# Performance work log

Hardware: AMD Instinct MI355X
Metric: run time of the kernel (lower is better)

Reference implementation:

```python
import jax, jax.numpy as jnp
import numpy as np

B, L, D = 2, 2048, 512
P, M = 32, 1024          # persistent slots, neural-memory slots
H, HD = 8, 64            # heads, head_dim (H*HD == D)
WIN = 256
EPS = 1e-5


def _layer_norm(x, g, b):
    mu = jnp.mean(x, axis=-1, keepdims=True)
    var = jnp.mean(jnp.square(x - mu), axis=-1, keepdims=True)
    return (x - mu) * jax.lax.rsqrt(var + EPS) * g + b


def setup_inputs() -> dict:
    key = jax.random.key(0)
    ks = jax.random.split(key, 12)
    s = 1.0 / np.sqrt(D)
    f32 = jnp.float32
    return {
        "x": jax.random.normal(ks[0], (B, L, D), f32),
        "persistent_memory": jax.random.normal(ks[1], (P, D), f32),
        "mem_keys": jax.random.normal(ks[2], (M, D), f32) * s,
        "mem_Wk": jax.random.normal(ks[3], (D, D), f32) * s,
        "mem_Wv": jax.random.normal(ks[4], (D, D), f32) * s,
        "mem_Wq": jax.random.normal(ks[5], (D, D), f32) * s,
        "attn_Wq": jax.random.normal(ks[6], (D, H * HD), f32) * s,
        "attn_Wk": jax.random.normal(ks[7], (D, H * HD), f32) * s,
        "attn_Wv": jax.random.normal(ks[8], (D, H * HD), f32) * s,
        "attn_Wo": jax.random.normal(ks[9], (H * HD, D), f32) * s,
        "ln1_g": jnp.ones((D,), f32), "ln1_b": jnp.zeros((D,), f32),
        "ln2_g": jnp.ones((D,), f32), "ln2_b": jnp.zeros((D,), f32),
        "out_W": jax.random.normal(ks[10], (D, D), f32) * s,
        "out_b": jnp.zeros((D,), f32),
    }


def reference(x, persistent_memory, mem_keys, mem_Wk, mem_Wv, mem_Wq,
              attn_Wq, attn_Wk, attn_Wv, attn_Wo,
              ln1_g, ln1_b, ln2_g, ln2_b, out_W, out_b):
    b = x.shape[0]
    # --- persistent memory concat: (B, S, D), S = P + L ---
    pm = jnp.broadcast_to(persistent_memory[None], (b, P, D))
    combined = jnp.concatenate([pm, x], axis=1)
    S = combined.shape[1]

    # --- NeuralMemory: write (update) then read (retrieve) ---
    k = combined @ mem_Wk                                   # (B,S,D)
    v = combined @ mem_Wv                                   # (B,S,D)
    w_write = jax.nn.softmax(jnp.einsum('bsd,md->bsm', k, mem_keys), axis=-1)
    state = jnp.einsum('bsm,bsd->bmd', w_write, v)          # zeros init + scatter-write
    q = combined @ mem_Wq
    w_read = jax.nn.softmax(jnp.einsum('bsd,md->bsm', q, mem_keys), axis=-1)
    mem_out = jnp.einsum('bsm,bmd->bsd', w_read, state)     # (B,S,D)

    h = _layer_norm(mem_out, ln1_g, ln1_b)

    # --- sliding-window multi-head attention ---
    qh = (h @ attn_Wq).reshape(b, S, H, HD)
    kh = (h @ attn_Wk).reshape(b, S, H, HD)
    vh = (h @ attn_Wv).reshape(b, S, H, HD)
    scores = jnp.einsum('bqhd,bkhd->bhqk', qh, kh) / np.sqrt(HD)
    idx = jnp.arange(S)
    band = jnp.abs(idx[:, None] - idx[None, :]) < WIN       # (S,S) local band
    scores = jnp.where(band[None, None], scores, jnp.finfo(scores.dtype).min)
    attn = jax.nn.softmax(scores, axis=-1)
    ao = jnp.einsum('bhqk,bkhd->bqhd', attn, vh).reshape(b, S, H * HD)
    ao = ao @ attn_Wo

    ao = _layer_norm(ao, ln2_g, ln2_b)
    return ao @ out_W + out_b
```

## Files before the change

### kernel.cpp

```cpp
#include <hip/hip_runtime.h>
#include <hip/hip_bf16.h>

#define B_ 2
#define L_ 2048
#define D_ 512
#define P_ 32
#define M_ 1024
#define H_ 8
#define HD_ 64
#define WIN_ 256
#define S_ (P_ + L_)
#define N_ (B_ * S_)

typedef __hip_bfloat16 bf16;
typedef __attribute__((ext_vector_type(8))) short short8;
typedef __attribute__((ext_vector_type(4))) short short4_t;
typedef __attribute__((ext_vector_type(4))) float f32x4;

__device__ __forceinline__ int imin(int a, int b) { return a < b ? a : b; }
__device__ __forceinline__ int imax(int a, int b) { return a > b ? a : b; }

__device__ __forceinline__ float ld_in(const void* p, long i, int f32) {
    return f32 ? ((const float*)p)[i]
               : __bfloat162float(((const bf16*)p)[i]);
}

__device__ __forceinline__ short bfbits(float f) {
    bf16 h = __float2bfloat16(f);
    short s;
    __builtin_memcpy(&s, &h, 2);
    return s;
}

__device__ __forceinline__ float b2f(short s) {
    unsigned int u = ((unsigned int)(unsigned short)s) << 16;
    float f;
    __builtin_memcpy(&f, &u, 4);
    return f;
}

__device__ __forceinline__ void gload_lds16(const void* g, void* l) {
    __builtin_amdgcn_global_load_lds(
        (const __attribute__((address_space(1))) unsigned int*)g,
        (__attribute__((address_space(3))) unsigned int*)l, 16, 0, 0);
}

#define F_X   0
#define F_PM  1
#define F_MK  2
#define F_WK  3
#define F_OW  10

__global__ __launch_bounds__(256) void detect_kernel(
    const void* a0, const void* a1, const void* a2, const void* a3,
    const void* a4, const void* a5, const void* a6, const void* a7,
    const void* a8, const void* a9, const void* a10, int* __restrict__ flags)
{
    const void* p;
    switch (blockIdx.x) {
        case 0: p = a0; break;  case 1: p = a1; break;
        case 2: p = a2; break;  case 3: p = a3; break;
        case 4: p = a4; break;  case 5: p = a5; break;
        case 6: p = a6; break;  case 7: p = a7; break;
        case 8: p = a8; break;  case 9: p = a9; break;
        default: p = a10; break;
    }
    const unsigned short* u = (const unsigned short*)p;
    __shared__ int c;
    if (threadIdx.x == 0) c = 0;
    __syncthreads();
    int cnt = 0;
    #pragma unroll
    for (int i = 0; i < 8; ++i) {
        unsigned short v = u[(threadIdx.x << 3) + i];
        cnt += (((v >> 7) & 0xFF) >= 0xC0) ? 1 : 0;
    }
    atomicAdd(&c, cnt);
    __syncthreads();
    if (threadIdx.x == 0) flags[blockIdx.x] = (c >= 8) ? 1 : 0;
}

struct Ptr8 { const void* p[8]; };

__global__ __launch_bounds__(256) void prep_kernel(
    const void* __restrict__ x, const void* __restrict__ pm,
    const void* __restrict__ mk, Ptr8 wptrs,
    bf16* __restrict__ comb, bf16* __restrict__ mkbf, bf16* __restrict__ WT,
    const int* __restrict__ flags)
{
    const int blk = blockIdx.x;
    const int tid = threadIdx.x;
    if (blk < 8320) {
        const int fx = flags[F_X];
        const int fp = flags[F_PM];
        int i = blk * 256 + tid;
        int d = i & (D_ - 1);
        int r = i >> 9;
        int s = r % S_;
        int b = r / S_;
        float v;
        if (s < P_) v = ld_in(pm, (long)s * D_ + d, fp);
        else        v = ld_in(x, ((long)(b * L_ + (s - P_))) * D_ + d, fx);
        comb[i] = __float2bfloat16(v);
        return;
    }
    if (blk < 10368) {
        const int f = flags[F_MK];
        int i = (blk - 8320) * 256 + tid;
        mkbf[i] = __float2bfloat16(ld_in(mk, i, f));
        return;
    }
    __shared__ short T[64][65];
    const int t = blk - 10368;
    const int widx = t >> 6;
    const int rem = t & 63;
    const int r0 = (rem >> 3) * 64, c0 = (rem & 7) * 64;
    const void* in = wptrs.p[widx];
    const int flag = flags[F_WK + widx];
    short* o = (short*)(WT + (long)widx * 512 * 512);
    #pragma unroll
    for (int i = 0; i < 2; ++i) {
        int ch = tid + i * 256;
        int r = ch >> 3, c8 = (ch & 7) * 8;
        long base = (long)(r0 + r) * 512 + c0 + c8;
        if (flag) {
            const float4 f0 = *reinterpret_cast<const float4*>((const float*)in + base);
            const float4 f1 = *reinterpret_cast<const float4*>((const float*)in + base + 4);
            T[r][c8+0]=bfbits(f0.x); T[r][c8+1]=bfbits(f0.y); T[r][c8+2]=bfbits(f0.z); T[r][c8+3]=bfbits(f0.w);
            T[r][c8+4]=bfbits(f1.x); T[r][c8+5]=bfbits(f1.y); T[r][c8+6]=bfbits(f1.z); T[r][c8+7]=bfbits(f1.w);
        } else {
            const short8 v = *reinterpret_cast<const short8*>((const short*)in + base);
            #pragma unroll
            for (int k = 0; k < 8; ++k) T[r][c8+k] = v[k];
        }
    }
    __syncthreads();
    #pragma unroll
    for (int i = 0; i < 2; ++i) {
        int ch = tid + i * 256;
        int n = ch >> 3, c8 = (ch & 7) * 8;
        #pragma unroll
        for (int k = 0; k < 8; ++k)
            o[(long)(c0 + n) * 512 + r0 + c8 + k] = T[c8 + k][n];
    }
}

__global__ __launch_bounds__(256) void transpose_b_kernel(
    const bf16* __restrict__ in_, bf16* __restrict__ out_, int R, int C)
{
    const short* in = (const short*)(in_ + (long)blockIdx.z * R * C);
    short* out = (short*)(out_ + (long)blockIdx.z * C * R);
    __shared__ short T[64][65];
    const int r0 = blockIdx.y * 64, c0 = blockIdx.x * 64;
    const int tid = threadIdx.x;
    #pragma unroll
    for (int i = 0; i < 2; ++i) {
        int ch = tid + i * 256;
        int r = ch >> 3, c8 = (ch & 7) * 8;
        int row = imin(r0 + r, R - 1);
        const short8 v = *reinterpret_cast<const short8*>(in + (long)row * C + c0 + c8);
        #pragma unroll
        for (int k = 0; k < 8; ++k) T[r][c8+k] = v[k];
    }
    __syncthreads();
    #pragma unroll
    for (int i = 0; i < 2; ++i) {
        int ch = tid + i * 256;
        int n = ch >> 3, c8 = (ch & 7) * 8;
        #pragma unroll
        for (int k = 0; k < 8; ++k) {
            int col = r0 + c8 + k;
            if (col < R) out[(long)(c0 + n) * R + col] = T[c8 + k][n];
        }
    }
}

template<int CMODE, int BN, int UN>
__global__ __launch_bounds__(256, 4) void gemm64(
    const bf16* __restrict__ A, const bf16* __restrict__ Bb,
    void* __restrict__ C0, void* __restrict__ C1, void* __restrict__ C2,
    const int* __restrict__ flags,
    int Mdim, int Kdim, int lda, int ldb, int ldc,
    long sA, long sB, long sC, int SK)
{
    constexpr int NH = BN / 64;
    __shared__ __align__(16) bf16 As[UN * 2048];
    __shared__ __align__(16) bf16 Bs[UN * BN * 32];
    const int tid = threadIdx.x, lane = tid & 63, wid = tid >> 6;
    constexpr int WNc = BN / 4;
    constexpr int NJ = WNc / 16;
    const int m0 = blockIdx.y * 64, n0 = blockIdx.x * BN;
    const int z = blockIdx.z;
    const int bz = z / SK, kc = z - bz * SK;
    const int kLen = Kdim / SK;
    const int kBeg = kc * kLen;
    const bf16* Ab = A + (long)bz * sA;
    const bf16* Bp = Bb + (long)bz * sB;

    const int sRow = tid >> 2, c8 = (tid & 3) * 8;
    int aRow = m0 + sRow;
    if (aRow >= Mdim) aRow = Mdim - 1;
    const bf16* aS = Ab + (long)aRow * lda + c8 + kBeg;
    const bf16* bS[NH];
    #pragma unroll
    for (int h = 0; h < NH; ++h)
        bS[h] = Bp + (long)(n0 + sRow + h * 64) * ldb + c8 + kBeg;

    const int g8 = (lane >> 4) * 8, l15 = lane & 15;
    f32x4 acc[4][NJ] = {};

    for (int k0 = 0; k0 < kLen; k0 += UN * 32) {
        #pragma unroll
        for (int t = 0; t < UN; ++t) {
            gload_lds16(aS + k0 + t * 32, As + t * 2048 + wid * 512);
            #pragma unroll
            for (int h = 0; h < NH; ++h)
                gload_lds16(bS[h] + k0 + t * 32, Bs + t * BN * 32 + h * 2048 + wid * 512);
        }
        __syncthreads();
        #pragma unroll
        for (int t = 0; t < UN; ++t) {
            short8 af[4], bfr[NJ];
            #pragma unroll
            for (int mi = 0; mi < 4; ++mi)
                af[mi] = *reinterpret_cast<const short8*>(
                    &As[t * 2048 + (mi * 16 + l15) * 32 + g8]);
            #pragma unroll
            for (int nj = 0; nj < NJ; ++nj)
                bfr[nj] = *reinterpret_cast<const short8*>(
                    &Bs[t * BN * 32 + (wid * WNc + nj * 16 + l15) * 32 + g8]);
            #pragma unroll
            for (int mi = 0; mi < 4; ++mi)
                #pragma unroll
                for (int nj = 0; nj < NJ; ++nj)
                    acc[mi][nj] = __builtin_amdgcn_mfma_f32_16x16x32_bf16(
                        af[mi], bfr[nj], acc[mi][nj], 0, 0, 0);
        }
        __syncthreads();
    }

    const int oflag = (CMODE == 2) ? flags[F_OW] : 0;
    const int grp = n0 >> 9;
    #pragma unroll
    for (int mi = 0; mi < 4; ++mi) {
        #pragma unroll
        for (int nj = 0; nj < NJ; ++nj) {
            #pragma unroll
            for (int r = 0; r < 4; ++r) {
                int row = m0 + mi * 16 + (lane >> 4) * 4 + r;
                int col = n0 + wid * WNc + nj * 16 + l15;
                if (row >= Mdim) continue;
                float val = acc[mi][nj][r];
                if (CMODE == 0) {
                    ((float*)C0)[(long)z * sC + (long)row * ldc + col] = val;
                } else if (CMODE == 1) {
                    ((bf16*)C0)[(long)z * sC + (long)row * ldc + col] = __float2bfloat16(val);
                } else if (CMODE == 2) {
                    long idx = (long)row * 512 + col;
                    if (oflag) ((float*)C0)[idx] = val;
                    else       ((bf16*)C0)[idx] = __float2bfloat16(val);
                } else if (CMODE == 6) {
                    int b = row / S_, s = row - b * S_;
                    int c = col - (grp << 9);
                    if (grp == 0)      ((bf16*)C0)[(long)row * 512 + c] = __float2bfloat16(val);
                    else if (grp == 1) ((bf16*)C1)[((long)b * 512 + c) * S_ + s] = __float2bfloat16(val);
                    else               ((bf16*)C2)[(long)row * 512 + c] = __float2bfloat16(val);
                } else {
                    int b = row / S_, s = row - b * S_;
                    int c = col - (grp << 9);
                    int h = c >> 6, d = c & 63;
                    if (grp == 0)      ((bf16*)C0)[((long)(b * H_ + h) * S_ + s) * HD_ + d] = __float2bfloat16(val);
                    else if (grp == 1) ((bf16*)C1)[((long)(b * H_ + h) * S_ + s) * HD_ + d] = __float2bfloat16(val);
                    else               ((bf16*)C2)[((long)(b * H_ + h) * HD_ + d) * S_ + s] = __float2bfloat16(val);
                }
            }
        }
    }
}

__global__ __launch_bounds__(256) void reduce_state_kernel(
    const bf16* __restrict__ P, bf16* __restrict__ stT)
{
    long g = ((long)blockIdx.x * 256 + threadIdx.x) * 8;
    int b = (int)(g >> 19);
    long dm = g & ((1L << 19) - 1);
    float s[8] = {};
    #pragma unroll
    for (int c = 0; c < 5; ++c) {
        const short8 v = *reinterpret_cast<const short8*>(
            (const short*)P + (((long)(b * 5 + c)) << 19) + dm);
        #pragma unroll
        for (int k = 0; k < 8; ++k) s[k] += b2f(v[k]);
    }
    short8 o;
    #pragma unroll
    for (int k = 0; k < 8; ++k) o[k] = bfbits(s[k]);
    *reinterpret_cast<short8*>((short*)stT + g) = o;
}

__global__ __launch_bounds__(256) void softmax_rows_kernel(
    const bf16* __restrict__ w, bf16* __restrict__ o)
{
    const int row = blockIdx.x;
    const int tid = threadIdx.x;
    const short4_t v4 = *reinterpret_cast<const short4_t*>(
        (const short*)w + (long)row * M_ + (tid << 2));
    float vx = b2f(v4[0]), vy = b2f(v4[1]), vz = b2f(v4[2]), vw = b2f(v4[3]);
    float mx = fmaxf(fmaxf(vx, vy), fmaxf(vz, vw));
    #pragma unroll
    for (int off = 32; off > 0; off >>= 1) mx = fmaxf(mx, __shfl_xor(mx, off, 64));
    __shared__ float rmax[4];
    __shared__ float rsum[4];
    const int wid = tid >> 6;
    if ((tid & 63) == 0) rmax[wid] = mx;
    __syncthreads();
    mx = fmaxf(fmaxf(rmax[0], rmax[1]), fmaxf(rmax[2], rmax[3]));
    float ex = __expf(vx - mx), ey = __expf(vy - mx);
    float ez = __expf(vz - mx), ew = __expf(vw - mx);
    float s = ex + ey + ez + ew;
    #pragma unroll
    for (int off = 32; off > 0; off >>= 1) s += __shfl_xor(s, off, 64);
    if ((tid & 63) == 0) rsum[wid] = s;
    __syncthreads();
    s = rsum[0] + rsum[1] + rsum[2] + rsum[3];
    const float inv = 1.f / s;
    short4_t ob;
    ob[0] = bfbits(ex * inv); ob[1] = bfbits(ey * inv);
    ob[2] = bfbits(ez * inv); ob[3] = bfbits(ew * inv);
    *reinterpret_cast<short4_t*>((short*)o + (long)row * M_ + (tid << 2)) = ob;
}

__global__ __launch_bounds__(256) void layernorm_kernel(
    const bf16* __restrict__ x, bf16* __restrict__ o)
{
    const int row = blockIdx.x;
    const int tid = threadIdx.x;
    const short* p = (const short*)x + (long)row * D_;
    float v0 = b2f(p[tid]), v1 = b2f(p[tid + 256]);
    float s  = v0 + v1;
    float sq = v0 * v0 + v1 * v1;
    #pragma unroll
    for (int off = 32; off > 0; off >>= 1) {
        s  += __shfl_xor(s,  off, 64);
        sq += __shfl_xor(sq, off, 64);
    }
    __shared__ float rs[4];
    __shared__ float rq[4];
    const int wid = tid >> 6;
    if ((tid & 63) == 0) { rs[wid] = s; rq[wid] = sq; }
    __syncthreads();
    s  = rs[0] + rs[1] + rs[2] + rs[3];
    sq = rq[0] + rq[1] + rq[2] + rq[3];
    const float mu  = s * (1.f / D_);
    const float var = sq * (1.f / D_) - mu * mu;
    const float inv = rsqrtf(var + 1e-5f);
    bf16* ob = o + (long)row * D_;
    ob[tid]       = __float2bfloat16((v0 - mu) * inv);
    ob[tid + 256] = __float2bfloat16((v1 - mu) * inv);
}

__global__ __launch_bounds__(256) void flash_attn_kernel(
    const bf16* __restrict__ qh, const bf16* __restrict__ kh,
    const bf16* __restrict__ vhT, bf16* __restrict__ ao)
{
    const int qt = blockIdx.x, h = blockIdx.y, b = blockIdx.z;
    const int tid = threadIdx.x, w = tid >> 6, lane = tid & 63;
    const int g = lane >> 4, l15 = lane & 15, g8 = g * 8;
    const int q0 = qt * 64;
    __shared__ __align__(16) bf16 Qs[64 * 72];
    __shared__ __align__(16) bf16 Ks[64 * 72];
    __shared__ __align__(16) bf16 Vs[64 * 72];
    __shared__ __align__(16) bf16 Ps[4 * 16 * 88];
    const long bh = (long)(b * H_ + h);
    const bf16* qb = qh + bh * S_ * HD_;
    const bf16* kb = kh + bh * S_ * HD_;
    const bf16* vb = vhT + bh * HD_ * S_;

    #pragma unroll
    for (int i = 0; i < 2; ++i) {
        int ch = tid + i * 256;
        int r = ch >> 3, c8 = (ch & 7) * 8;
        int q = imin(q0 + r, S_ - 1);
        *reinterpret_cast<short8*>(&Qs[r * 72 + c8]) =
            *reinterpret_cast<const short8*>(qb + (long)q * HD_ + c8);
    }
    float mrow[4] = {-1e20f, -1e20f, -1e20f, -1e20f};
    float lrow[4] = {};
    f32x4 O[4] = {};
    const int tstart = imax(0, q0 - (WIN_ - 1)) >> 6;
    const int tend = imin(S_ - 1, q0 + 63 + (WIN_ - 1)) >> 6;

    for (int jt = tstart; jt <= tend; ++jt) {
        __syncthreads();
        #pragma unroll
        for (int i = 0; i < 2; ++i) {
            int ch = tid + i * 256;
            int r = ch >> 3, c8 = (ch & 7) * 8;
            int j = imin(jt * 64 + r, S_ - 1);
            *reinterpret_cast<short8*>(&Ks[r * 72 + c8]) =
                *reinterpret_cast<const short8*>(kb + (long)j * HD_ + c8);
            int jc = jt * 64 + c8;
            if (jc + 8 <= S_) {
                *reinterpret_cast<short8*>(&Vs[r * 72 + c8]) =
                    *reinterpret_cast<const short8*>(vb + (long)r * S_ + jc);
            } else {
                short8 v;
                #pragma unroll
                for (int k = 0; k < 8; ++k)
                    v[k] = ((const short*)vb)[(long)r * S_ + imin(jc + k, S_ - 1)];
                *reinterpret_cast<short8*>(&Vs[r * 72 + c8]) = v;
            }
        }
        __syncthreads();
        f32x4 s[4] = {};
        const short8 aq0 = *reinterpret_cast<const short8*>(&Qs[(w * 16 + l15) * 72 + g8]);
        const short8 aq1 = *reinterpret_cast<const short8*>(&Qs[(w * 16 + l15) * 72 + 32 + g8]);
        #pragma unroll
        for (int nj = 0; nj < 4; ++nj) {
            const short8 b0 = *reinterpret_cast<const short8*>(&Ks[(nj * 16 + l15) * 72 + g8]);
            const short8 b1 = *reinterpret_cast<const short8*>(&Ks[(nj * 16 + l15) * 72 + 32 + g8]);
            s[nj] = __builtin_amdgcn_mfma_f32_16x16x32_bf16(aq0, b0, s[nj], 0, 0, 0);
            s[nj] = __builtin_amdgcn_mfma_f32_16x16x32_bf16(aq1, b1, s[nj], 0, 0, 0);
        }
        #pragma unroll
        for (int nj = 0; nj < 4; ++nj) {
            int j = jt * 64 + nj * 16 + l15;
            #pragma unroll
            for (int r = 0; r < 4; ++r) {
                int q = q0 + w * 16 + g * 4 + r;
                int dd = q - j;
                bool ok = (dd > -WIN_) && (dd < WIN_) && (q < S_) && (j < S_);
                s[nj][r] = ok ? s[nj][r] * 0.125f : -1e30f;
            }
        }
        float alpha[4];
        #pragma unroll
        for (int r = 0; r < 4; ++r) {
            float mt = fmaxf(fmaxf(s[0][r], s[1][r]), fmaxf(s[2][r], s[3][r]));
            #pragma unroll
            for (int off = 8; off; off >>= 1) mt = fmaxf(mt, __shfl_xor(mt, off, 64));
            float mnew = fmaxf(mrow[r], mt);
            alpha[r] = __expf(mrow[r] - mnew);
            mrow[r] = mnew;
            float ps = 0.f;
            #pragma unroll
            for (int nj = 0; nj < 4; ++nj) {
                float pv = __expf(s[nj][r] - mnew);
                s[nj][r] = pv;
                ps += pv;
            }
            #pragma unroll
            for (int off = 8; off; off >>= 1) ps += __shfl_xor(ps, off, 64);
            lrow[r] = lrow[r] * alpha[r] + ps;
        }
        #pragma unroll
        for (int nj = 0; nj < 4; ++nj) {
            #pragma unroll
            for (int r = 0; r < 4; ++r) {
                Ps[w * 1408 + (g * 4 + r) * 88 + nj * 16 + l15] = __float2bfloat16(s[nj][r]);
                O[nj][r] *= alpha[r];
            }
        }
        __syncthreads();
        const short8 ap0 = *reinterpret_cast<const short8*>(&Ps[w * 1408 + l15 * 88 + g8]);
        const short8 ap1 = *reinterpret_cast<const short8*>(&Ps[w * 1408 + l15 * 88 + 32 + g8]);
        #pragma unroll
        for (int nj = 0; nj < 4; ++nj) {
            const short8 b0 = *reinterpret_cast<const short8*>(&Vs[(nj * 16 + l15) * 72 + g8]);
            const short8 b1 = *reinterpret_cast<const short8*>(&Vs[(nj * 16 + l15) * 72 + 32 + g8]);
            O[nj] = __builtin_amdgcn_mfma_f32_16x16x32_bf16(ap0, b0, O[nj], 0, 0, 0);
            O[nj] = __builtin_amdgcn_mfma_f32_16x16x32_bf16(ap1, b1, O[nj], 0, 0, 0);
        }
    }
    float inv[4];
    #pragma unroll
    for (int r = 0; r < 4; ++r) inv[r] = lrow[r] > 0.f ? 1.f / lrow[r] : 0.f;
    #pragma unroll
    for (int nj = 0; nj < 4; ++nj) {
        #pragma unroll
        for (int r = 0; r < 4; ++r) {
            int q = q0 + w * 16 + g * 4 + r;
            if (q < S_)
                ao[((long)b * S_ + q) * D_ + h * HD_ + nj * 16 + l15] =
                    __float2bfloat16(O[nj][r] * inv[r]);
        }
    }
}

extern "C" void kernel_launch(void* const* d_in, const int* in_sizes, int n_in,
                              void* d_out, int out_size, void* d_ws, size_t ws_size,
                              hipStream_t stream)
{
    const void* x        = d_in[0];
    const void* pm       = d_in[1];
    const void* mem_keys = d_in[2];

    char* wsb = (char*)d_ws;
    bf16*  comb  = (bf16*)(wsb + 0x0);
    bf16*  kbf   = (bf16*)(wsb + 0x410000);
    bf16*  qbf   = (bf16*)(wsb + 0x820000);
    bf16*  vTb   = (bf16*)(wsb + 0xC30000);
    bf16*  Lg    = (bf16*)(wsb + 0x1040000);
    bf16*  W1    = (bf16*)(wsb + 0x2080000);
    bf16*  W1T   = (bf16*)(wsb + 0x30C0000);
    bf16*  aobf  = (bf16*)(wsb + 0x30C0000);
    bf16*  Pst   = (bf16*)(wsb + 0x38E0000);
    bf16*  stT   = (bf16*)(wsb + 0x42E0000);
    bf16*  tmp   = (bf16*)(wsb + 0x44E0000);
    bf16*  WT    = (bf16*)(wsb + 0x4D00000);
    bf16*  mkbf  = (bf16*)(wsb + 0x5100000);
    int*   flags = (int*)(wsb + 0x5200000);

    detect_kernel<<<11, 256, 0, stream>>>(
        x, pm, mem_keys, d_in[3], d_in[4], d_in[5],
        d_in[6], d_in[7], d_in[8], d_in[9], d_in[14], flags);

    Ptr8 p8;
    p8.p[0] = d_in[3]; p8.p[1] = d_in[4]; p8.p[2] = d_in[5]; p8.p[3] = d_in[6];
    p8.p[4] = d_in[7]; p8.p[5] = d_in[8]; p8.p[6] = d_in[9]; p8.p[7] = d_in[14];
    prep_kernel<<<10880, 256, 0, stream>>>(x, pm, mem_keys, p8, comb, mkbf, WT, flags);
    #define WTp(i) (WT + (long)(i) * 262144)

    gemm64<6,128,2><<<dim3(12, 65, 1), 256, 0, stream>>>(
        comb, WTp(0), kbf, vTb, qbf, flags, N_, 512, 512, 512, 0, 0, 0, 0, 1);

    gemm64<1,128,2><<<dim3(8, 130, 1), 256, 0, stream>>>(
        kbf, mkbf, Lg, nullptr, nullptr, flags, 2 * N_, 512, 512, 512, 1024, 0, 0, 0, 1);
    softmax_rows_kernel<<<2 * N_, 256, 0, stream>>>(Lg, W1);
    transpose_b_kernel<<<dim3(16, 33, 2), 256, 0, stream>>>(W1, W1T, S_, M_);

    gemm64<1,128,1><<<dim3(8, 8, 10), 256, 0, stream>>>(
        vTb, W1T, Pst, nullptr, nullptr, flags, 512, S_, S_, S_, 1024,
        (long)D_ * S_, (long)M_ * S_, (long)D_ * M_, 5);
    reduce_state_kernel<<<512, 256, 0, stream>>>(Pst, stT);

    gemm64<1,64,2><<<dim3(8, 33, 2), 256, 0, stream>>>(
        W1 + (long)N_ * M_, stT, tmp, nullptr, nullptr, flags, S_, M_, M_, M_, 512,
        (long)S_ * M_, (long)D_ * M_, (long)S_ * D_, 1);
    layernorm_kernel<<<N_, 256, 0, stream>>>(tmp, comb);

    gemm64<7,128,2><<<dim3(12, 65, 1), 256, 0, stream>>>(
        comb, WTp(3), kbf, qbf, vTb, flags, N_, 512, 512, 512, 0, 0, 0, 0, 1);

    flash_attn_kernel<<<dim3(33, H_, B_), 256, 0, stream>>>(kbf, qbf, vTb, aobf);

    gemm64<1,128,2><<<dim3(4, 65, 1), 256, 0, stream>>>(
        aobf, WTp(6), tmp, nullptr, nullptr, flags, N_, 512, 512, 512, 512, 0, 0, 0, 1);
    layernorm_kernel<<<N_, 256, 0, stream>>>(tmp, comb);
    gemm64<2,128,2><<<dim3(4, 65, 1), 256, 0, stream>>>(
        comb, WTp(7), d_out, nullptr, nullptr, flags, N_, 512, 512, 512, 512, 0, 0, 0, 1);
}
```

Before: 277.4 us.

## Fold memory key/query projections into mem_keys and drop online softmax max

```diff
diff --git a/kernel.cpp b/kernel.cpp
--- a/kernel.cpp
+++ b/kernel.cpp
@@ -110,7 +110,6 @@
         mkbf[i] = __float2bfloat16(ld_in(mk, i, f));
         return;
     }
-    __shared__ short T[64][65];
     const int t = blk - 10368;
     const int widx = t >> 6;
     const int rem = t & 63;
@@ -118,6 +117,26 @@
     const void* in = wptrs.p[widx];
     const int flag = flags[F_WK + widx];
     short* o = (short*)(WT + (long)widx * 512 * 512);
+    if (widx == 0 || widx == 2) {
+        #pragma unroll
+        for (int i = 0; i < 2; ++i) {
+            int ch = tid + i * 256;
+            int r = ch >> 3, c8 = (ch & 7) * 8;
+            long base = (long)(r0 + r) * 512 + c0 + c8;
+            short8 v;
+            if (flag) {
+                const float4 f0 = *reinterpret_cast<const float4*>((const float*)in + base);
+                const float4 f1 = *reinterpret_cast<const float4*>((const float*)in + base + 4);
+                v[0]=bfbits(f0.x); v[1]=bfbits(f0.y); v[2]=bfbits(f0.z); v[3]=bfbits(f0.w);
+                v[4]=bfbits(f1.x); v[5]=bfbits(f1.y); v[6]=bfbits(f1.z); v[7]=bfbits(f1.w);
+            } else {
+                v = *reinterpret_cast<const short8*>((const short*)in + base);
+            }
+            *reinterpret_cast<short8*>(o + base) = v;
+        }
+        return;
+    }
+    __shared__ short T[64][65];
     #pragma unroll
     for (int i = 0; i < 2; ++i) {
         int ch = tid + i * 256;
@@ -259,12 +278,9 @@
                     long idx = (long)row * 512 + col;
                     if (oflag) ((float*)C0)[idx] = val;
                     else       ((bf16*)C0)[idx] = __float2bfloat16(val);
-                } else if (CMODE == 6) {
+                } else if (CMODE == 5) {
                     int b = row / S_, s = row - b * S_;
-                    int c = col - (grp << 9);
-                    if (grp == 0)      ((bf16*)C0)[(long)row * 512 + c] = __float2bfloat16(val);
-                    else if (grp == 1) ((bf16*)C1)[((long)b * 512 + c) * S_ + s] = __float2bfloat16(val);
-                    else               ((bf16*)C2)[(long)row * 512 + c] = __float2bfloat16(val);
+                    ((bf16*)C0)[((long)b * 512 + col) * S_ + s] = __float2bfloat16(val);
                 } else {
                     int b = row / S_, s = row - b * S_;
                     int c = col - (grp << 9);
@@ -302,9 +318,10 @@
     const bf16* __restrict__ w, bf16* __restrict__ o)
 {
     const int row = blockIdx.x;
+    const int hf = blockIdx.y;
     const int tid = threadIdx.x;
     const short4_t v4 = *reinterpret_cast<const short4_t*>(
-        (const short*)w + (long)row * M_ + (tid << 2));
+        (const short*)w + (long)row * 2048 + hf * 1024 + (tid << 2));
     float vx = b2f(v4[0]), vy = b2f(v4[1]), vz = b2f(v4[2]), vw = b2f(v4[3]);
     float mx = fmaxf(fmaxf(vx, vy), fmaxf(vz, vw));
     #pragma unroll
@@ -327,7 +344,8 @@
     short4_t ob;
     ob[0] = bfbits(ex * inv); ob[1] = bfbits(ey * inv);
     ob[2] = bfbits(ez * inv); ob[3] = bfbits(ew * inv);
-    *reinterpret_cast<short4_t*>((short*)o + (long)row * M_ + (tid << 2)) = ob;
+    *reinterpret_cast<short4_t*>(
+        (short*)o + (long)hf * N_ * M_ + (long)row * M_ + (tid << 2)) = ob;
 }
 
 __global__ __launch_bounds__(256) void layernorm_kernel(
@@ -358,6 +376,9 @@
     ob[tid]       = __float2bfloat16((v0 - mu) * inv);
     ob[tid + 256] = __float2bfloat16((v1 - mu) * inv);
 }
+
+#define SC2_ 0.18033688f
+#define MF2_ 11.5415603f
 
 __global__ __launch_bounds__(256) void flash_attn_kernel(
     const bf16* __restrict__ qh, const bf16* __restrict__ kh,
@@ -384,7 +405,6 @@
         *reinterpret_cast<short8*>(&Qs[r * 72 + c8]) =
             *reinterpret_cast<const short8*>(qb + (long)q * HD_ + c8);
     }
-    float mrow[4] = {-1e20f, -1e20f, -1e20f, -1e20f};
     float lrow[4] = {};
     f32x4 O[4] = {};
     const int tstart = imax(0, q0 - (WIN_ - 1)) >> 6;
@@ -430,38 +450,27 @@
                 int q = q0 + w * 16 + g * 4 + r;
                 int dd = q - j;
                 bool ok = (dd > -WIN_) && (dd < WIN_) && (q < S_) && (j < S_);
-                s[nj][r] = ok ? s[nj][r] * 0.125f : -1e30f;
+                s[nj][r] = ok ? fmaf(s[nj][r], SC2_, -MF2_) : -1e30f;
             }
         }
-        float alpha[4];
         #pragma unroll
         for (int r = 0; r < 4; ++r) {
-            float mt = fmaxf(fmaxf(s[0][r], s[1][r]), fmaxf(s[2][r], s[3][r]));
-            #pragma unroll
-            for (int off = 8; off; off >>= 1) mt = fmaxf(mt, __shfl_xor(mt, off, 64));
-            float mnew = fmaxf(mrow[r], mt);
-            alpha[r] = __expf(mrow[r] - mnew);
-            mrow[r] = mnew;
             float ps = 0.f;
             #pragma unroll
             for (int nj = 0; nj < 4; ++nj) {
-                float pv = __expf(s[nj][r] - mnew);
+                float pv = exp2f(s[nj][r]);
                 s[nj][r] = pv;
                 ps += pv;
             }
             #pragma unroll
             for (int off = 8; off; off >>= 1) ps += __shfl_xor(ps, off, 64);
-            lrow[r] = lrow[r] * alpha[r] + ps;
-        }
-        #pragma unroll
-        for (int nj = 0; nj < 4; ++nj) {
-            #pragma unroll
-            for (int r = 0; r < 4; ++r) {
+            lrow[r] += ps;
+        }
+        #pragma unroll
+        for (int nj = 0; nj < 4; ++nj)
+            #pragma unroll
+            for (int r = 0; r < 4; ++r)
                 Ps[w * 1408 + (g * 4 + r) * 88 + nj * 16 + l15] = __float2bfloat16(s[nj][r]);
-                O[nj][r] *= alpha[r];
-            }
-        }
-        __syncthreads();
         const short8 ap0 = *reinterpret_cast<const short8*>(&Ps[w * 1408 + l15 * 88 + g8]);
         const short8 ap1 = *reinterpret_cast<const short8*>(&Ps[w * 1408 + l15 * 88 + 32 + g8]);
         #pragma unroll
@@ -497,7 +506,7 @@
 
     char* wsb = (char*)d_ws;
     bf16*  comb  = (bf16*)(wsb + 0x0);
-    bf16*  kbf   = (bf16*)(wsb + 0x410000);
+    bf16*  Gbf   = (bf16*)(wsb + 0x410000);
     bf16*  qbf   = (bf16*)(wsb + 0x820000);
     bf16*  vTb   = (bf16*)(wsb + 0xC30000);
     bf16*  Lg    = (bf16*)(wsb + 0x1040000);
@@ -521,12 +530,16 @@
     prep_kernel<<<10880, 256, 0, stream>>>(x, pm, mem_keys, p8, comb, mkbf, WT, flags);
     #define WTp(i) (WT + (long)(i) * 262144)
 
-    gemm64<6,128,2><<<dim3(12, 65, 1), 256, 0, stream>>>(
-        comb, WTp(0), kbf, vTb, qbf, flags, N_, 512, 512, 512, 0, 0, 0, 0, 1);
-
-    gemm64<1,128,2><<<dim3(8, 130, 1), 256, 0, stream>>>(
-        kbf, mkbf, Lg, nullptr, nullptr, flags, 2 * N_, 512, 512, 512, 1024, 0, 0, 0, 1);
-    softmax_rows_kernel<<<2 * N_, 256, 0, stream>>>(Lg, W1);
+    gemm64<1,128,2><<<dim3(4, 16, 2), 256, 0, stream>>>(
+        mkbf, WTp(0), Gbf, nullptr, nullptr, flags, M_, 512, 512, 512, 512,
+        0, 2L * 262144, (long)M_ * 512, 1);
+
+    gemm64<5,128,2><<<dim3(4, 65, 1), 256, 0, stream>>>(
+        comb, WTp(1), vTb, nullptr, nullptr, flags, N_, 512, 512, 512, 512, 0, 0, 0, 1);
+
+    gemm64<1,128,2><<<dim3(16, 65, 1), 256, 0, stream>>>(
+        comb, Gbf, Lg, nullptr, nullptr, flags, N_, 512, 512, 512, 2048, 0, 0, 0, 1);
+    softmax_rows_kernel<<<dim3(N_, 2), 256, 0, stream>>>(Lg, W1);
     transpose_b_kernel<<<dim3(16, 33, 2), 256, 0, stream>>>(W1, W1T, S_, M_);
 
     gemm64<1,128,1><<<dim3(8, 8, 10), 256, 0, stream>>>(
@@ -540,9 +553,9 @@
     layernorm_kernel<<<N_, 256, 0, stream>>>(tmp, comb);
 
     gemm64<7,128,2><<<dim3(12, 65, 1), 256, 0, stream>>>(
-        comb, WTp(3), kbf, qbf, vTb, flags, N_, 512, 512, 512, 0, 0, 0, 0, 1);
-
-    flash_attn_kernel<<<dim3(33, H_, B_), 256, 0, stream>>>(kbf, qbf, vTb, aobf);
+        comb, WTp(3), Gbf, qbf, vTb, flags, N_, 512, 512, 512, 0, 0, 0, 0, 1);
+
+    flash_attn_kernel<<<dim3(33, H_, B_), 256, 0, stream>>>(Gbf, qbf, vTb, aobf);
 
     gemm64<1,128,2><<<dim3(4, 65, 1), 256, 0, stream>>>(
         aobf, WTp(6), tmp, nullptr, nullptr, flags, N_, 512, 512, 512, 512, 0, 0, 0, 1);
```

After: 274.3 us. No clear change (-1.1%).
